# Kernel tuning notes

Measured on AMD Instinct MI355X. Metric: run time of the kernel, lower is better.

The kernel has to match this reference:

```python
import jax, jax.numpy as jnp
import numpy as np

IN_DIM = 1024
OUT_DIM = 65536
BATCH = 32
MASK_DENSITY = 0.1  # fraction of weights kept, mimicking LSH neuron selection


def setup_inputs() -> dict:
    key = jax.random.key(0)
    kx, kw, km = jax.random.split(key, 3)
    x = jax.random.normal(kx, (BATCH, IN_DIM), dtype=jnp.float32)
    w = jax.random.normal(kw, (IN_DIM, OUT_DIM), dtype=jnp.float32) * 0.05
    mask = (jax.random.uniform(km, (IN_DIM, OUT_DIM)) < MASK_DENSITY).astype(jnp.float32)
    b = jnp.zeros((OUT_DIM,), dtype=jnp.float32)
    return {"x": x, "mask": mask, "w": w, "b": b}


def reference(x, mask, w, b):
    # Faithful math of: sparse_dense_matmul(x, from_dense(w * squeeze(mask))) + b
    # which is exactly x @ (w * mask) + b in dense form.
    masked_w = w * mask  # [in, out]
    return jnp.matmul(x, masked_w) + b  # [batch, out]
```

## Files before the change

### kernel.cpp

```cpp
#include <hip/hip_runtime.h>


#define IN_DIM 1024
#define OUT_DIM 65536
#define BATCH 32
#define KSPLIT 4
#define KCHUNK (IN_DIM / KSPLIT)
#define BLOCK 256
#define U 8
#define NG (KCHUNK / U)

template <bool ATOMIC>
__global__ __launch_bounds__(BLOCK, 4) void sl_partial(
    const float* __restrict__ x, const float* __restrict__ mask,
    const float* __restrict__ w, float* __restrict__ dst) {
  __shared__ float xT[KCHUNK * BATCH];
  const int tid = threadIdx.x;
  const int j = blockIdx.x * BLOCK + tid;
  const int kc = blockIdx.y;
  const int k0 = kc * KCHUNK;

#pragma unroll
  for (int it = 0; it < (KCHUNK * BATCH) / BLOCK; ++it) {
    int idx = it * BLOCK + tid;
    int kl = idx & (KCHUNK - 1);
    int i = idx >> 8;
    xT[kl * BATCH + i] = x[i * IN_DIM + k0 + kl];
  }
  __syncthreads();

  float acc[BATCH];
#pragma unroll
  for (int i = 0; i < BATCH; ++i) acc[i] = 0.0f;

  const float* wp = w + (size_t)k0 * OUT_DIM + j;
  const float* mp = mask + (size_t)k0 * OUT_DIM + j;

  float wA[U], mA[U], wB[U], mB[U];

  auto loadg = [&](int g, float* wv, float* mv) {
#pragma unroll
    for (int u = 0; u < U; ++u) {
      size_t off = (size_t)(g * U + u) * OUT_DIM;
      wv[u] = __builtin_nontemporal_load(wp + off);
      mv[u] = __builtin_nontemporal_load(mp + off);
    }
  };
  auto computeg = [&](int g, const float* wv, const float* mv) {
#pragma unroll
    for (int u = 0; u < U; ++u) {
      float wm = wv[u] * mv[u];
      const float4* xp = (const float4*)&xT[(g * U + u) * BATCH];
#pragma unroll
      for (int i4 = 0; i4 < BATCH / 4; ++i4) {
        float4 q = xp[i4];
        acc[i4 * 4 + 0] = fmaf(q.x, wm, acc[i4 * 4 + 0]);
        acc[i4 * 4 + 1] = fmaf(q.y, wm, acc[i4 * 4 + 1]);
        acc[i4 * 4 + 2] = fmaf(q.z, wm, acc[i4 * 4 + 2]);
        acc[i4 * 4 + 3] = fmaf(q.w, wm, acc[i4 * 4 + 3]);
      }
    }
  };

  loadg(0, wA, mA);
#pragma unroll 1
  for (int g = 0; g < NG; g += 2) {
    loadg(g + 1, wB, mB);
    computeg(g, wA, mA);
    if (g + 2 < NG) loadg(g + 2, wA, mA);
    computeg(g + 1, wB, mB);
  }

  if (ATOMIC) {
#pragma unroll
    for (int i = 0; i < BATCH; ++i)
      atomicAdd(dst + (size_t)i * OUT_DIM + j, acc[i]);
  } else {
#pragma unroll
    for (int i = 0; i < BATCH; ++i)
      __builtin_nontemporal_store(
          acc[i], dst + (size_t)(kc * BATCH + i) * OUT_DIM + j);
  }
}

__global__ __launch_bounds__(BLOCK) void sl_reduce(
    const float* __restrict__ ws, const float* __restrict__ b,
    float* __restrict__ out) {
  const int j4 = blockIdx.x * BLOCK + threadIdx.x;
  const int i = blockIdx.y;
  const float4 bv = ((const float4*)b)[j4];
  float4 s = bv;
#pragma unroll
  for (int kc = 0; kc < KSPLIT; ++kc) {
    float4 p = ((const float4*)ws)[(size_t)(kc * BATCH + i) * (OUT_DIM / 4) + j4];
    s.x += p.x;
    s.y += p.y;
    s.z += p.z;
    s.w += p.w;
  }
  ((float4*)out)[(size_t)i * (OUT_DIM / 4) + j4] = s;
}

__global__ __launch_bounds__(BLOCK) void sl_init(
    const float* __restrict__ b, float* __restrict__ out) {
  const int j4 = blockIdx.x * BLOCK + threadIdx.x;
  const float4 bv = ((const float4*)b)[j4];
#pragma unroll
  for (int i = 0; i < BATCH; ++i)
    ((float4*)out)[(size_t)i * (OUT_DIM / 4) + j4] = bv;
}

extern "C" void kernel_launch(void* const* d_in, const int* in_sizes, int n_in,
                              void* d_out, int out_size, void* d_ws, size_t ws_size,
                              hipStream_t stream) {
  const float* x = (const float*)d_in[0];
  const float* mask = (const float*)d_in[1];
  const float* w = (const float*)d_in[2];
  const float* b = (const float*)d_in[3];
  float* out = (float*)d_out;

  const size_t need = (size_t)KSPLIT * BATCH * OUT_DIM * sizeof(float);
  if (ws_size >= need) {
    hipLaunchKernelGGL((sl_partial<false>), dim3(OUT_DIM / BLOCK, KSPLIT),
                       dim3(BLOCK), 0, stream, x, mask, w, (float*)d_ws);
    hipLaunchKernelGGL(sl_reduce, dim3(OUT_DIM / 4 / BLOCK, BATCH), dim3(BLOCK),
                       0, stream, (const float*)d_ws, b, out);
  } else {
    hipLaunchKernelGGL(sl_init, dim3(OUT_DIM / 4 / BLOCK), dim3(BLOCK), 0,
                       stream, b, out);
    hipLaunchKernelGGL((sl_partial<true>), dim3(OUT_DIM / BLOCK, KSPLIT),
                       dim3(BLOCK), 0, stream, x, mask, w, out);
  }
}
```

Before: 504.0 us.

## Vectorize weight/mask loads to float4 per thread with wider register tile

Each thread now computes four adjacent output columns using 128-bit loads of w and mask and a 32x4 accumulator tile. This cuts the number of load instructions and reuses each shared-memory x value across four columns. To keep enough blocks, the K split is raised from 4 to 8 and the unroll depth reduced. The cost is a larger workspace and reduce pass (twice the partial sums) and higher register pressure, now with a launch bound of two blocks per CU.

```diff
diff --git a/kernel.cpp b/kernel.cpp
--- a/kernel.cpp
+++ b/kernel.cpp
@@ -4,19 +4,22 @@
 #define IN_DIM 1024
 #define OUT_DIM 65536
 #define BATCH 32
-#define KSPLIT 4
+#define KSPLIT 8
 #define KCHUNK (IN_DIM / KSPLIT)
 #define BLOCK 256
-#define U 8
+#define U 2
 #define NG (KCHUNK / U)
+#define OUT4 (OUT_DIM / 4)
+
+typedef float f4 __attribute__((ext_vector_type(4)));
 
 template <bool ATOMIC>
-__global__ __launch_bounds__(BLOCK, 4) void sl_partial(
+__global__ __launch_bounds__(BLOCK, 2) void sl_partial_v4(
     const float* __restrict__ x, const float* __restrict__ mask,
     const float* __restrict__ w, float* __restrict__ dst) {
   __shared__ float xT[KCHUNK * BATCH];
   const int tid = threadIdx.x;
-  const int j = blockIdx.x * BLOCK + tid;
+  const int j4 = blockIdx.x * BLOCK + tid;
   const int kc = blockIdx.y;
   const int k0 = kc * KCHUNK;
 
@@ -24,40 +27,52 @@
   for (int it = 0; it < (KCHUNK * BATCH) / BLOCK; ++it) {
     int idx = it * BLOCK + tid;
     int kl = idx & (KCHUNK - 1);
-    int i = idx >> 8;
+    int i = idx >> 7;
     xT[kl * BATCH + i] = x[i * IN_DIM + k0 + kl];
   }
   __syncthreads();
 
-  float acc[BATCH];
+  f4 acc[BATCH];
 #pragma unroll
-  for (int i = 0; i < BATCH; ++i) acc[i] = 0.0f;
+  for (int i = 0; i < BATCH; ++i) acc[i] = (f4)(0.0f);
 
-  const float* wp = w + (size_t)k0 * OUT_DIM + j;
-  const float* mp = mask + (size_t)k0 * OUT_DIM + j;
+  const f4* wp = (const f4*)w + (size_t)k0 * OUT4 + j4;
+  const f4* mp = (const f4*)mask + (size_t)k0 * OUT4 + j4;
 
-  float wA[U], mA[U], wB[U], mB[U];
+  f4 wA[U], mA[U], wB[U], mB[U];
 
-  auto loadg = [&](int g, float* wv, float* mv) {
+  auto loadg = [&](int g, f4* wv, f4* mv) {
 #pragma unroll
     for (int u = 0; u < U; ++u) {
-      size_t off = (size_t)(g * U + u) * OUT_DIM;
+      size_t off = (size_t)(g * U + u) * OUT4;
       wv[u] = __builtin_nontemporal_load(wp + off);
       mv[u] = __builtin_nontemporal_load(mp + off);
     }
   };
-  auto computeg = [&](int g, const float* wv, const float* mv) {
+  auto computeg = [&](int g, const f4* wv, const f4* mv) {
 #pragma unroll
     for (int u = 0; u < U; ++u) {
-      float wm = wv[u] * mv[u];
-      const float4* xp = (const float4*)&xT[(g * U + u) * BATCH];
+      f4 wm = wv[u] * mv[u];
+      const f4* xp = (const f4*)&xT[(g * U + u) * BATCH];
 #pragma unroll
       for (int i4 = 0; i4 < BATCH / 4; ++i4) {
-        float4 q = xp[i4];
-        acc[i4 * 4 + 0] = fmaf(q.x, wm, acc[i4 * 4 + 0]);
-        acc[i4 * 4 + 1] = fmaf(q.y, wm, acc[i4 * 4 + 1]);
-        acc[i4 * 4 + 2] = fmaf(q.z, wm, acc[i4 * 4 + 2]);
-        acc[i4 * 4 + 3] = fmaf(q.w, wm, acc[i4 * 4 + 3]);
+        f4 q = xp[i4];
+        acc[i4 * 4 + 0].x = fmaf(q.x, wm.x, acc[i4 * 4 + 0].x);
+        acc[i4 * 4 + 0].y = fmaf(q.x, wm.y, acc[i4 * 4 + 0].y);
+        acc[i4 * 4 + 0].z = fmaf(q.x, wm.z, acc[i4 * 4 + 0].z);
+        acc[i4 * 4 + 0].w = fmaf(q.x, wm.w, acc[i4 * 4 + 0].w);
+        acc[i4 * 4 + 1].x = fmaf(q.y, wm.x, acc[i4 * 4 + 1].x);
+        acc[i4 * 4 + 1].y = fmaf(q.y, wm.y, acc[i4 * 4 + 1].y);
+        acc[i4 * 4 + 1].z = fmaf(q.y, wm.z, acc[i4 * 4 + 1].z);
+        acc[i4 * 4 + 1].w = fmaf(q.y, wm.w, acc[i4 * 4 + 1].w);
+        acc[i4 * 4 + 2].x = fmaf(q.z, wm.x, acc[i4 * 4 + 2].x);
+        acc[i4 * 4 + 2].y = fmaf(q.z, wm.y, acc[i4 * 4 + 2].y);
+        acc[i4 * 4 + 2].z = fmaf(q.z, wm.z, acc[i4 * 4 + 2].z);
+        acc[i4 * 4 + 2].w = fmaf(q.z, wm.w, acc[i4 * 4 + 2].w);
+        acc[i4 * 4 + 3].x = fmaf(q.w, wm.x, acc[i4 * 4 + 3].x);
+        acc[i4 * 4 + 3].y = fmaf(q.w, wm.y, acc[i4 * 4 + 3].y);
+        acc[i4 * 4 + 3].z = fmaf(q.w, wm.z, acc[i4 * 4 + 3].z);
+        acc[i4 * 4 + 3].w = fmaf(q.w, wm.w, acc[i4 * 4 + 3].w);
       }
     }
   };
@@ -73,13 +88,18 @@
 
   if (ATOMIC) {
 #pragma unroll
-    for (int i = 0; i < BATCH; ++i)
-      atomicAdd(dst + (size_t)i * OUT_DIM + j, acc[i]);
+    for (int i = 0; i < BATCH; ++i) {
+      float* d = dst + (size_t)i * OUT_DIM + j4 * 4;
+      atomicAdd(d + 0, acc[i].x);
+      atomicAdd(d + 1, acc[i].y);
+      atomicAdd(d + 2, acc[i].z);
+      atomicAdd(d + 3, acc[i].w);
+    }
   } else {
+    f4* wsp = (f4*)dst;
 #pragma unroll
     for (int i = 0; i < BATCH; ++i)
-      __builtin_nontemporal_store(
-          acc[i], dst + (size_t)(kc * BATCH + i) * OUT_DIM + j);
+      wsp[(size_t)(kc * BATCH + i) * OUT4 + j4] = acc[i];
   }
 }
 
@@ -88,26 +108,22 @@
     float* __restrict__ out) {
   const int j4 = blockIdx.x * BLOCK + threadIdx.x;
   const int i = blockIdx.y;
-  const float4 bv = ((const float4*)b)[j4];
-  float4 s = bv;
+  f4 s = ((const f4*)b)[j4];
 #pragma unroll
   for (int kc = 0; kc < KSPLIT; ++kc) {
-    float4 p = ((const float4*)ws)[(size_t)(kc * BATCH + i) * (OUT_DIM / 4) + j4];
-    s.x += p.x;
-    s.y += p.y;
-    s.z += p.z;
-    s.w += p.w;
+    f4 p = ((const f4*)ws)[(size_t)(kc * BATCH + i) * OUT4 + j4];
+    s += p;
   }
-  ((float4*)out)[(size_t)i * (OUT_DIM / 4) + j4] = s;
+  ((f4*)out)[(size_t)i * OUT4 + j4] = s;
 }
 
 __global__ __launch_bounds__(BLOCK) void sl_init(
     const float* __restrict__ b, float* __restrict__ out) {
   const int j4 = blockIdx.x * BLOCK + threadIdx.x;
-  const float4 bv = ((const float4*)b)[j4];
+  const f4 bv = ((const f4*)b)[j4];
 #pragma unroll
   for (int i = 0; i < BATCH; ++i)
-    ((float4*)out)[(size_t)i * (OUT_DIM / 4) + j4] = bv;
+    ((f4*)out)[(size_t)i * OUT4 + j4] = bv;
 }
 
 extern "C" void kernel_launch(void* const* d_in, const int* in_sizes, int n_in,
@@ -121,14 +137,14 @@
 
   const size_t need = (size_t)KSPLIT * BATCH * OUT_DIM * sizeof(float);
   if (ws_size >= need) {
-    hipLaunchKernelGGL((sl_partial<false>), dim3(OUT_DIM / BLOCK, KSPLIT),
+    hipLaunchKernelGGL((sl_partial_v4<false>), dim3(OUT4 / BLOCK, KSPLIT),
                        dim3(BLOCK), 0, stream, x, mask, w, (float*)d_ws);
-    hipLaunchKernelGGL(sl_reduce, dim3(OUT_DIM / 4 / BLOCK, BATCH), dim3(BLOCK),
-                       0, stream, (const float*)d_ws, b, out);
+    hipLaunchKernelGGL(sl_reduce, dim3(OUT4 / BLOCK, BATCH), dim3(BLOCK), 0,
+                       stream, (const float*)d_ws, b, out);
   } else {
-    hipLaunchKernelGGL(sl_init, dim3(OUT_DIM / 4 / BLOCK), dim3(BLOCK), 0,
-                       stream, b, out);
-    hipLaunchKernelGGL((sl_partial<true>), dim3(OUT_DIM / BLOCK, KSPLIT),
+    hipLaunchKernelGGL(sl_init, dim3(OUT4 / BLOCK), dim3(BLOCK), 0, stream, b,
+                       out);
+    hipLaunchKernelGGL((sl_partial_v4<true>), dim3(OUT4 / BLOCK, KSPLIT),
                        dim3(BLOCK), 0, stream, x, mask, w, out);
   }
 }
```

Measured after the change: 517.2 us. +2.6%, slower.
